# Kernel optimization log

Measured on AMD Instinct MI355X. Metric: run time of the kernel, lower is better.

The kernel has to match this reference:

```python
import jax, jax.numpy as jnp
import numpy as np
from jax import lax

TAU_MEM = 100.0   # 1/0.01 default
V_LEAK = 0.0
V_TH = 1.0


def setup_inputs() -> dict:
    key = jax.random.key(0)
    k1, k2 = jax.random.split(key)
    B, T, F = 32, 128, 2048
    inp = jax.random.normal(k1, (B, T, F), dtype=jnp.float32)
    W = jax.random.normal(k2, (F, F), dtype=jnp.float32) * (1.0 / np.sqrt(F))
    b = jnp.zeros((F,), dtype=jnp.float32)
    return {"input": inp, "W": W, "b": b}


def _heaviside(x):
    return (x > 0).astype(x.dtype)


def reference(input, W, b):
    # time-distributed kernel: Linear applied to all timesteps at once
    gs = jnp.einsum('btn,mn->btm', input, W) + b  # [B, T, F]
    dt_over_tau = 1.0 / TAU_MEM

    def step(v, g):
        # Euler LIF update with delta (subtractive) reset
        v_new = v + dt_over_tau * ((V_LEAK - v) + g)
        z = _heaviside(v_new - V_TH)
        v_reset = v_new - z * V_TH
        return v_reset, z

    v0 = jnp.zeros(gs.shape[::2], dtype=gs.dtype)  # [B, F]
    _, zs = lax.scan(step, v0, jnp.moveaxis(gs, 1, 0))  # zs: [T, B, F]
    return jnp.moveaxis(zs, 0, 1)  # [B, T, F]
```

## Files before the change

### kernel.cpp

```cpp
#include <hip/hip_runtime.h>
#include <hip/hip_bf16.h>
#include <stdint.h>

#define Bdim 32
#define Tdim 128
#define Fdim 2048
#define Mdim (Bdim*Tdim)

#define BM 128
#define BN 128
#define BK 64

typedef __attribute__((ext_vector_type(8))) short bf16x8;
typedef __attribute__((ext_vector_type(4))) float f32x4;

__device__ inline unsigned short f2bf(float f) {
    union { float f; unsigned u; } x; x.f = f;
    unsigned r = (x.u + 0x7fffu + ((x.u >> 16) & 1u)) >> 16;
    return (unsigned short)r;
}

__global__ void convert_kernel(const float* __restrict__ A, const float* __restrict__ W,
                               unsigned short* __restrict__ a16, unsigned short* __restrict__ w16) {
    const int nA4 = (Mdim * Fdim) / 4;
    const int nW4 = (Fdim * Fdim) / 4;
    const int stride = gridDim.x * blockDim.x;
    for (int i = blockIdx.x * blockDim.x + threadIdx.x; i < nA4 + nW4; i += stride) {
        const float4* src; unsigned short* dst; int j;
        if (i < nA4) { src = (const float4*)A; dst = a16; j = i; }
        else         { src = (const float4*)W; dst = w16; j = i - nA4; }
        float4 v = src[j];
        ushort4 o;
        o.x = f2bf(v.x); o.y = f2bf(v.y); o.z = f2bf(v.z); o.w = f2bf(v.w);
        *(ushort4*)(dst + 4 * (size_t)j) = o;
    }
}

__global__ __launch_bounds__(256) void gemm_kernel(const unsigned short* __restrict__ A,
                                                   const unsigned short* __restrict__ Wm,
                                                   float* __restrict__ C) {
    __shared__ __align__(16) unsigned short sA[2][BM * BK];
    __shared__ __align__(16) unsigned short sB[2][BN * BK];

    const int tid = threadIdx.x;
    const int wid = tid >> 6, lane = tid & 63;
    const int wr = wid >> 1, wc = wid & 1;
    const int m0 = blockIdx.y * BM, n0 = blockIdx.x * BN;

    f32x4 acc[4][4];
#pragma unroll
    for (int i = 0; i < 4; i++)
#pragma unroll
        for (int j = 0; j < 4; j++) acc[i][j] = f32x4{0.f, 0.f, 0.f, 0.f};

    const int frow = lane & 15;
    const int lgrp = lane >> 4;

    auto stage = [&](int buf, int kt) {
        const int k0 = kt * BK;
#pragma unroll
        for (int j = 0; j < 4; ++j) {
            const int base = wid * 1024 + j * 4096;
            const int off  = base + lane * 16;
            const int row  = off >> 7;
            const int chk  = (off & 127) >> 4;
            const int scol = ((chk ^ (row & 7)) << 3);
            const unsigned short* ga = A  + (size_t)(m0 + row) * Fdim + k0 + scol;
            const unsigned short* gb = Wm + (size_t)(n0 + row) * Fdim + k0 + scol;
            __builtin_amdgcn_global_load_lds(
                (const __attribute__((address_space(1))) void*)ga,
                (__attribute__((address_space(3))) void*)((char*)&sA[buf][0] + base),
                16, 0, 0);
            __builtin_amdgcn_global_load_lds(
                (const __attribute__((address_space(1))) void*)gb,
                (__attribute__((address_space(3))) void*)((char*)&sB[buf][0] + base),
                16, 0, 0);
        }
    };

    stage(0, 0);
    __syncthreads();

    int cur = 0;
    const int NT = Fdim / BK;
    for (int kt = 0; kt < NT; ++kt) {
        if (kt + 1 < NT) stage(cur ^ 1, kt + 1);

        bf16x8 af[2][4], bfr[2][4];
#pragma unroll
        for (int kk = 0; kk < 2; kk++) {
            const int chunk = kk * 4 + lgrp;
#pragma unroll
            for (int mi = 0; mi < 4; mi++) {
                const int r = wr * 64 + mi * 16 + frow;
                af[kk][mi] = *(const bf16x8*)(&sA[cur][0] + r * BK + ((chunk ^ (r & 7)) << 3));
            }
#pragma unroll
            for (int ni = 0; ni < 4; ni++) {
                const int r = wc * 64 + ni * 16 + frow;
                bfr[kk][ni] = *(const bf16x8*)(&sB[cur][0] + r * BK + ((chunk ^ (r & 7)) << 3));
            }
        }
#pragma unroll
        for (int kk = 0; kk < 2; kk++)
#pragma unroll
            for (int mi = 0; mi < 4; mi++)
#pragma unroll
                for (int ni = 0; ni < 4; ni++)
                    acc[mi][ni] = __builtin_amdgcn_mfma_f32_16x16x32_bf16(af[kk][mi], bfr[kk][ni], acc[mi][ni], 0, 0, 0);

        __syncthreads();
        cur ^= 1;
    }

    const int crow = m0 + wr * 64 + (lane >> 4) * 4;
    const int ccol = n0 + wc * 64 + (lane & 15);
#pragma unroll
    for (int mi = 0; mi < 4; mi++)
#pragma unroll
        for (int ni = 0; ni < 4; ni++) {
            float* cp = C + (size_t)(crow + mi * 16) * Fdim + ccol + ni * 16;
#pragma unroll
            for (int r = 0; r < 4; r++) cp[(size_t)r * Fdim] = acc[mi][ni][r];
        }
}

__global__ void gemm_f32_naive(const float* __restrict__ A, const float* __restrict__ W,
                               float* __restrict__ C) {
    int col = blockIdx.x * blockDim.x + threadIdx.x;
    int row = blockIdx.y;
    float s = 0.f;
    for (int k = 0; k < Fdim; k++) s += A[(size_t)row * Fdim + k] * W[(size_t)col * Fdim + k];
    C[(size_t)row * Fdim + col] = s;
}

__global__ __launch_bounds__(256, 1) void lif_kernel(float* __restrict__ gs,
                                                     const float* __restrict__ bias) {
    int idx = blockIdx.x * blockDim.x + threadIdx.x;
    int b = idx >> 11, f = idx & (Fdim - 1);
    const float bf = bias[f];
    float* p = gs + (size_t)b * Tdim * Fdim + f;

    float g[Tdim];
#pragma unroll
    for (int t = 0; t < Tdim; t++) g[t] = p[(size_t)t * Fdim];

    float v = 0.f;
#pragma unroll
    for (int t = 0; t < Tdim; t++) {
        float vn = v + 0.01f * ((0.0f - v) + (g[t] + bf));
        float z = (vn > 1.0f) ? 1.0f : 0.0f;
        v = vn - z;
        p[(size_t)t * Fdim] = z;
    }
}

extern "C" void kernel_launch(void* const* d_in, const int* in_sizes, int n_in,
                              void* d_out, int out_size, void* d_ws, size_t ws_size,
                              hipStream_t stream) {
    const float* inp  = (const float*)d_in[0];
    const float* W    = (const float*)d_in[1];
    const float* bias = (const float*)d_in[2];
    float* out = (float*)d_out;

    const size_t needA = (size_t)Mdim * Fdim * 2;
    const size_t needW = (size_t)Fdim * Fdim * 2;

    if (ws_size >= needA + needW) {
        unsigned short* a16 = (unsigned short*)d_ws;
        unsigned short* w16 = (unsigned short*)((char*)d_ws + needA);
        convert_kernel<<<2048, 256, 0, stream>>>(inp, W, a16, w16);
        dim3 grid(Fdim / BN, Mdim / BM);
        gemm_kernel<<<grid, 256, 0, stream>>>(a16, w16, out);
    } else {
        dim3 grid(Fdim / 256, Mdim);
        gemm_f32_naive<<<grid, 256, 0, stream>>>(inp, W, out);
    }
    lif_kernel<<<(Bdim * Fdim) / 256, 256, 0, stream>>>(out, bias);
}
```

Baseline: 165.2 us.

## Fuse LIF recurrence into GEMM epilogue via shared-memory tile

```diff
diff --git a/kernel.cpp b/kernel.cpp
--- a/kernel.cpp
+++ b/kernel.cpp
@@ -36,11 +36,11 @@
     }
 }
 
-__global__ __launch_bounds__(256) void gemm_kernel(const unsigned short* __restrict__ A,
-                                                   const unsigned short* __restrict__ Wm,
-                                                   float* __restrict__ C) {
-    __shared__ __align__(16) unsigned short sA[2][BM * BK];
-    __shared__ __align__(16) unsigned short sB[2][BN * BK];
+__global__ __launch_bounds__(256) void gemm_fused_kernel(const unsigned short* __restrict__ A,
+                                                         const unsigned short* __restrict__ Wm,
+                                                         const float* __restrict__ bias,
+                                                         float* __restrict__ Z) {
+    __shared__ __align__(16) char smem[128 * 132 * 4];
 
     const int tid = threadIdx.x;
     const int wid = tid >> 6, lane = tid & 63;
@@ -58,6 +58,8 @@
 
     auto stage = [&](int buf, int kt) {
         const int k0 = kt * BK;
+        char* sAb = smem + buf * 16384;
+        char* sBb = smem + 32768 + buf * 16384;
 #pragma unroll
         for (int j = 0; j < 4; ++j) {
             const int base = wid * 1024 + j * 4096;
@@ -69,12 +71,10 @@
             const unsigned short* gb = Wm + (size_t)(n0 + row) * Fdim + k0 + scol;
             __builtin_amdgcn_global_load_lds(
                 (const __attribute__((address_space(1))) void*)ga,
-                (__attribute__((address_space(3))) void*)((char*)&sA[buf][0] + base),
-                16, 0, 0);
+                (__attribute__((address_space(3))) void*)(sAb + base), 16, 0, 0);
             __builtin_amdgcn_global_load_lds(
                 (const __attribute__((address_space(1))) void*)gb,
-                (__attribute__((address_space(3))) void*)((char*)&sB[buf][0] + base),
-                16, 0, 0);
+                (__attribute__((address_space(3))) void*)(sBb + base), 16, 0, 0);
         }
     };
 
@@ -86,6 +86,8 @@
     for (int kt = 0; kt < NT; ++kt) {
         if (kt + 1 < NT) stage(cur ^ 1, kt + 1);
 
+        const unsigned short* sAc = (const unsigned short*)(smem + cur * 16384);
+        const unsigned short* sBc = (const unsigned short*)(smem + 32768 + cur * 16384);
         bf16x8 af[2][4], bfr[2][4];
 #pragma unroll
         for (int kk = 0; kk < 2; kk++) {
@@ -93,12 +95,12 @@
 #pragma unroll
             for (int mi = 0; mi < 4; mi++) {
                 const int r = wr * 64 + mi * 16 + frow;
-                af[kk][mi] = *(const bf16x8*)(&sA[cur][0] + r * BK + ((chunk ^ (r & 7)) << 3));
+                af[kk][mi] = *(const bf16x8*)(sAc + r * BK + ((chunk ^ (r & 7)) << 3));
             }
 #pragma unroll
             for (int ni = 0; ni < 4; ni++) {
                 const int r = wc * 64 + ni * 16 + frow;
-                bfr[kk][ni] = *(const bf16x8*)(&sB[cur][0] + r * BK + ((chunk ^ (r & 7)) << 3));
+                bfr[kk][ni] = *(const bf16x8*)(sBc + r * BK + ((chunk ^ (r & 7)) << 3));
             }
         }
 #pragma unroll
@@ -113,16 +115,32 @@
         cur ^= 1;
     }
 
-    const int crow = m0 + wr * 64 + (lane >> 4) * 4;
-    const int ccol = n0 + wc * 64 + (lane & 15);
+    float* ct = (float*)smem;
 #pragma unroll
     for (int mi = 0; mi < 4; mi++)
 #pragma unroll
         for (int ni = 0; ni < 4; ni++) {
-            float* cp = C + (size_t)(crow + mi * 16) * Fdim + ccol + ni * 16;
+            const int r0 = wr * 64 + mi * 16 + (lane >> 4) * 4;
+            const int c0 = wc * 64 + ni * 16 + (lane & 15);
 #pragma unroll
-            for (int r = 0; r < 4; r++) cp[(size_t)r * Fdim] = acc[mi][ni][r];
+            for (int r = 0; r < 4; r++) ct[(r0 + r) * 132 + c0] = acc[mi][ni][r];
         }
+    __syncthreads();
+
+    if (tid < 128) {
+        const int gcol = n0 + tid;
+        const float bf = bias[gcol];
+        float* outp = Z + (size_t)m0 * Fdim + gcol;
+        float v = 0.f;
+#pragma unroll 16
+        for (int t = 0; t < Tdim; t++) {
+            const float g = ct[t * 132 + tid] + bf;
+            const float vn = v + 0.01f * ((0.0f - v) + g);
+            const float z = (vn > 1.0f) ? 1.0f : 0.0f;
+            v = vn - z;
+            outp[(size_t)t * Fdim] = z;
+        }
+    }
 }
 
 __global__ void gemm_f32_naive(const float* __restrict__ A, const float* __restrict__ W,
@@ -140,15 +158,11 @@
     int b = idx >> 11, f = idx & (Fdim - 1);
     const float bf = bias[f];
     float* p = gs + (size_t)b * Tdim * Fdim + f;
-
-    float g[Tdim];
-#pragma unroll
-    for (int t = 0; t < Tdim; t++) g[t] = p[(size_t)t * Fdim];
-
     float v = 0.f;
-#pragma unroll
+#pragma unroll 16
     for (int t = 0; t < Tdim; t++) {
-        float vn = v + 0.01f * ((0.0f - v) + (g[t] + bf));
+        float g = p[(size_t)t * Fdim] + bf;
+        float vn = v + 0.01f * ((0.0f - v) + g);
         float z = (vn > 1.0f) ? 1.0f : 0.0f;
         v = vn - z;
         p[(size_t)t * Fdim] = z;
@@ -171,10 +185,10 @@
         unsigned short* w16 = (unsigned short*)((char*)d_ws + needA);
         convert_kernel<<<2048, 256, 0, stream>>>(inp, W, a16, w16);
         dim3 grid(Fdim / BN, Mdim / BM);
-        gemm_kernel<<<grid, 256, 0, stream>>>(a16, w16, out);
+        gemm_fused_kernel<<<grid, 256, 0, stream>>>(a16, w16, bias, out);
     } else {
         dim3 grid(Fdim / 256, Mdim);
         gemm_f32_naive<<<grid, 256, 0, stream>>>(inp, W, out);
+        lif_kernel<<<(Bdim * Fdim) / 256, 256, 0, stream>>>(out, bias);
     }
-    lif_kernel<<<(Bdim * Fdim) / 256, 256, 0, stream>>>(out, bias);
 }
```

Result: faster. 139.8 us (-15.4%).
